# Performance work log

Hardware: AMD Instinct MI355X
Metric: run time of the kernel (lower is better)

Reference implementation:

```python
import jax, jax.numpy as jnp
import numpy as np

IMG_W, IMG_H = 640, 360
STRIDE = 32
S = 72                      # n_offsets
FMAP_H, FMAP_W = IMG_H // STRIDE, IMG_W // STRIDE   # 11, 20
CF = 64                     # anchor_feat_channels
CBACK = 512                 # resnet34 output channels
NP = 4                      # n_proposal
B = 512
F = CF * FMAP_H             # 704


def setup_inputs() -> dict:
    key = jax.random.key(0)
    ks = jax.random.split(key, 8)
    feat = jax.random.normal(ks[0], (B, CBACK, FMAP_H, FMAP_W), dtype=jnp.float32)
    # rpn proposals: (x_px, y_px, unused, angle_deg)
    x = jax.random.uniform(ks[1], (B, NP)) * IMG_W
    y = jax.random.uniform(ks[2], (B, NP)) * IMG_H
    ang = 30.0 + jax.random.uniform(ks[3], (B, NP)) * 120.0   # degrees in [30,150]
    rpn_proposals = jnp.stack([x, y, jnp.zeros_like(x), ang], axis=-1).astype(jnp.float32)
    conv_w = jax.random.normal(ks[4], (CF, CBACK), dtype=jnp.float32) * 0.02
    conv_b = jnp.zeros((CF,), jnp.float32)
    att_w = jax.random.normal(ks[5], (NP - 1, F), dtype=jnp.float32) * 0.02
    att_b = jnp.zeros((NP - 1,), jnp.float32)
    cls_w = jax.random.normal(ks[6], (2, 2 * F), dtype=jnp.float32) * 0.02
    cls_b = jnp.zeros((2,), jnp.float32)
    reg_w = jax.random.normal(ks[7], (S + 1, 2 * F), dtype=jnp.float32) * 0.02
    reg_b = jnp.zeros((S + 1,), jnp.float32)
    return {"feat": feat, "rpn_proposals": rpn_proposals, "conv_w": conv_w,
            "conv_b": conv_b, "att_w": att_w, "att_b": att_b,
            "cls_w": cls_w, "cls_b": cls_b, "reg_w": reg_w, "reg_b": reg_b}


# off-diagonal scatter pattern of the 4x4 attention matrix (row-major order of eye==0)
_ROWS = np.repeat(np.arange(NP), NP - 1)                       # (12,)
_COLS = np.array([j for i in range(NP) for j in range(NP) if j != i])  # (12,)


def reference(feat, rpn_proposals, conv_w, conv_b, att_w, att_b, cls_w, cls_b, reg_w, reg_b):
    bsz = feat.shape[0]
    anchor_ys = jnp.linspace(1.0, 0.0, S)          # (72,)
    anchor_cut_ys = jnp.linspace(1.0, 0.0, FMAP_H) # (11,)

    # --- generate_anchor (vectorized over batch x 4 proposals) ---
    start_x = rpn_proposals[..., 0] / IMG_W        # (B,4)
    start_y = rpn_proposals[..., 1] / IMG_H        # (B,4)
    tan = jnp.tan(rpn_proposals[..., 3] * (np.pi / 180.0))
    xs_full = (start_x[..., None] + (start_y[..., None] - anchor_ys) / tan[..., None]) * IMG_W      # (B,4,72)
    xs_cut = (start_x[..., None] + (start_y[..., None] - anchor_cut_ys) / tan[..., None]) * IMG_W   # (B,4,11)

    anchors = jnp.zeros((bsz, NP, 5 + S), jnp.float32)
    anchors = anchors.at[..., 2].set(1.0 - start_y)
    anchors = anchors.at[..., 3].set(start_x)
    anchors = anchors.at[..., 5:].set(xs_full)

    # --- anchor cut indices (flip along fmap_h like the original) ---
    unclamped = jnp.flip(jnp.round(xs_cut / STRIDE).astype(jnp.int32), axis=-1)  # (B,4,11)
    cut_x = jnp.clip(unclamped, 0, FMAP_W - 1)
    invalid = (unclamped < 0) | (unclamped > FMAP_W)   # faithful: > fmap_w, not >=

    # --- conv1 (1x1 conv) ---
    f = jnp.einsum('bchw,oc->bohw', feat, conv_w) + conv_b[None, :, None, None]  # (B,64,11,20)

    # --- cut_anchor_features: gather f[b, c, y, cut_x[b,p,y]], zero invalid ---
    g = jnp.take_along_axis(f[:, None], cut_x[:, :, None, :, None], axis=4)[..., 0]  # (B,4,64,11)
    g = jnp.where(invalid[:, :, None, :], 0.0, g)
    anchor_feat = g.reshape(bsz, NP, F)  # (B,4,704)

    # --- attention: softmax over 3 non-self anchors, scattered off-diagonal ---
    scores = anchor_feat.reshape(-1, F) @ att_w.T + att_b          # (B*4,3)
    attention = jax.nn.softmax(scores, axis=1).reshape(bsz, NP, NP - 1)
    att_mat = jnp.zeros((bsz, NP, NP), jnp.float32).at[:, _ROWS, _COLS].set(attention.reshape(bsz, -1))

    # attention_features[b,i,:] = sum_j att_mat[b,i,j] * anchor_feat[b,j,:]
    att_feat = jnp.einsum('bij,bjf->bif', att_mat, anchor_feat)    # (B,4,704)
    cat = jnp.concatenate([att_feat, anchor_feat], axis=-1)        # (B,4,1408)

    cls_logits = cat @ cls_w.T + cls_b                             # (B,4,2)
    reg = cat @ reg_w.T + reg_b                                    # (B,4,73)

    reg_proposals = anchors
    reg_proposals = reg_proposals.at[..., :2].set(cls_logits)
    reg_proposals = reg_proposals.at[..., 4:].add(reg)
    # nms(): with conf_threshold=None, anchors[:,:,0]==0 so num_to_keep==4 -> all kept.
    return reg_proposals
```

## Files before the change

### kernel.cpp

```cpp
#include <hip/hip_runtime.h>
#include <math.h>

#define NPROP 4
#define SFULL 72
#define FH 11
#define FW 20
#define CB 512
#define FDIM 704
#define HW 220
#define CHT 32
#define NTILE 16
#define MROWS 160

typedef __attribute__((ext_vector_type(8))) short bf16x8;
typedef __attribute__((ext_vector_type(4))) float f32x4;

__device__ __forceinline__ unsigned short f2bf(float x) {
  unsigned u = __float_as_uint(x);
  u += 0x7FFFu + ((u >> 16) & 1u);
  return (unsigned short)(u >> 16);
}
__device__ __forceinline__ unsigned bfbits(float x) {
  unsigned u = __float_as_uint(x);
  return u + 0x7FFFu + ((u >> 16) & 1u);
}

__device__ __forceinline__ void gload16(const void* g, void* l) {
  __builtin_amdgcn_global_load_lds(
      (const __attribute__((address_space(1))) void*)(g),
      (__attribute__((address_space(3))) void*)(l), 16, 0, 0);
}

__global__ void k_prep(const float* __restrict__ cls_w, const float* __restrict__ reg_w,
                       const float* __restrict__ att_w, const float* __restrict__ conv_w,
                       unsigned short* __restrict__ Wc, unsigned short* __restrict__ Wb2) {
  const int blk = blockIdx.x;
  const int t = threadIdx.x;
  if (blk < MROWS) {
    const int m = blk;
    const float* rowp = nullptr;
    if (m < 150) {
      int o = (m < 75) ? m : m - 75;
      int half = (m < 75) ? 0 : FDIM;
      rowp = ((o < 2) ? (cls_w + o * 2 * FDIM) : (reg_w + (o - 2) * 2 * FDIM)) + half;
    } else if (m < 153) {
      rowp = att_w + (m - 150) * FDIM;
    }
    for (int f = t; f < FDIM; f += 256) {
      float v = rowp ? rowp[f] : 0.0f;
      int fp = (f % FH) * 64 + (f / FH);
      Wc[m * FDIM + fp] = f2bf(v);
    }
  } else {
    const int kg = blk - MROWS;
    #pragma unroll
    for (int e0 = 0; e0 < 2; e0++) {
      int e = t + 256 * e0;
      Wb2[kg * 512 + e] = f2bf(conv_w[(e >> 3) * CB + kg * 8 + (e & 7)]);
    }
  }
}

__global__ __launch_bounds__(512, 4) void k_gconv(
    const float* __restrict__ feat, const float* __restrict__ rpn,
    const unsigned short* __restrict__ Wb2, const float* __restrict__ conv_b,
    unsigned short* __restrict__ af, float* __restrict__ xs_full,
    float* __restrict__ out)
{
  __shared__ __align__(16) unsigned short W2[64 * 512];
  __shared__ __align__(16) unsigned short As[2 * 48 * 40];
  __shared__ float sh_sx[NPROP], sh_sy[NPROP], sh_it[NPROP];
  __shared__ int   sh_pos[48];
  __shared__ int   hcnt[55];
  __shared__ unsigned hword[55];

  const int b = blockIdx.x;
  const int t = threadIdx.x;
  const int l = t & 63;
  const int wid = t >> 6;
  const int nt = wid & 3;
  const int mhalf = wid >> 2;
  const int q = l >> 4, r = l & 15;

  if (t < NPROP) {
    const float* rp = rpn + (b * NPROP + t) * 4;
    float sx = rp[0] * (1.0f / 640.0f);
    float sy = rp[1] * (1.0f / 360.0f);
    float tn = tanf(rp[3] * 0.017453292519943295f);
    sh_sx[t] = sx; sh_sy[t] = sy; sh_it[t] = 1.0f / tn;
    out[(b * NPROP + t) * 77 + 2] = 1.0f - sy;
    out[(b * NPROP + t) * 77 + 3] = sx;
  }
  __syncthreads();
  if (t < NPROP * SFULL) {
    int p = t / SFULL, i = t - p * SFULL;
    float ay = 1.0f - (float)i * (1.0f / 71.0f);
    xs_full[(b * NPROP + p) * SFULL + i] =
        (sh_sx[p] + (sh_sy[p] - ay) * sh_it[p]) * 640.0f;
  }
  if (t < 48) {
    int ps = -1;
    if (t < NPROP * FH) {
      int p = t / FH, y = t - p * FH;
      float acy = 1.0f - (float)(10 - y) * 0.1f;
      float xc = (sh_sx[p] + (sh_sy[p] - acy) * sh_it[p]) * 640.0f;
      int ui = (int)rintf(xc * (1.0f / 32.0f));
      int cut = min(max(ui, 0), FW - 1);
      ps = ((ui < 0) | (ui > FW)) ? -1 : (t % FH) * FW + cut;
    }
    sh_pos[t] = ps;
  }
  __syncthreads();

  if (t < 55) {
    int cnt = 0; unsigned w = 0;
    for (int s = 0; s < 44; s++) {
      int p = sh_pos[s];
      if (p >= 0 && (p >> 2) == t) {
        w |= ((unsigned)(s | ((p & 3) << 6))) << (8 * cnt);
        cnt++;
      }
    }
    hcnt[t] = cnt; hword[t] = w;
  }
  __syncthreads();

  int hn[4]; unsigned hwd[4]; int chS[4]; int cid[4];
  const int cbase = 220 * wid;
  #pragma unroll
  for (int k = 0; k < 4; k++) {
    int c = cbase + 64 * k + l;
    bool ok = (k < 3) || (l < 28);
    cid[k] = c;
    int j = c % 55;
    chS[k] = c / 55;
    hn[k]  = ok ? hcnt[j] : 0;
    hwd[k] = hword[j];
  }

  const float* fb = feat + (size_t)b * (CB * HW);

  #pragma unroll
  for (int k = 0; k < 8; k++) {
    int chunk = t + 512 * k;
    gload16(Wb2 + chunk * 8, (void*)&W2[chunk * 8]);
  }
  __builtin_amdgcn_sched_barrier(0);

  float4 pf[3][4];
  #pragma unroll
  for (int s = 0; s < 3; s++) {
    const float4* g = (const float4*)(fb + s * (CHT * HW));
    #pragma unroll
    for (int k = 0; k < 3; k++) pf[s][k] = g[cid[k]];
    if (l < 28) pf[s][3] = g[cid[3]];
    __builtin_amdgcn_sched_barrier(0);
  }

  f32x4 acc0 = {0.f, 0.f, 0.f, 0.f}, acc1 = {0.f, 0.f, 0.f, 0.f};
  const int cW = 16 * nt + r;

  #pragma unroll
  for (int ct = 0; ct < NTILE; ct++) {
    if (ct <= 13)      asm volatile("s_waitcnt vmcnt(8)" ::: "memory");
    else if (ct == 14) asm volatile("s_waitcnt vmcnt(4)" ::: "memory");
    else               asm volatile("s_waitcnt vmcnt(0)" ::: "memory");
    __builtin_amdgcn_sched_barrier(0);

    unsigned short* Asb = As + (ct & 1) * 1920;
    #pragma unroll
    for (int k = 0; k < 4; k++) {
      int n = hn[k];
      if (n) {
        float4 v4 = pf[ct % 3][k];
        unsigned d0 = (bfbits(v4.x) >> 16) | (bfbits(v4.y) & 0xFFFF0000u);
        unsigned d1 = (bfbits(v4.z) >> 16) | (bfbits(v4.w) & 0xFFFF0000u);
        unsigned wd = hwd[k];
        #pragma unroll
        for (int h = 0; h < 4; h++) {
          if (h < n) {
            unsigned byte = (wd >> (8 * h)) & 255u;
            unsigned s = byte & 63u;
            unsigned sel = (byte & 128u) ? d1 : d0;
            unsigned short val = (byte & 64u) ? (unsigned short)(sel >> 16)
                                              : (unsigned short)sel;
            Asb[s * 40 + chS[k]] = val;
          }
        }
      }
    }
    if (ct + 3 < NTILE) {
      const float4* g = (const float4*)(fb + (ct + 3) * (CHT * HW));
      #pragma unroll
      for (int k = 0; k < 3; k++) pf[ct % 3][k] = g[cid[k]];
      if (l < 28) pf[ct % 3][3] = g[cid[3]];
    }
    asm volatile("s_waitcnt lgkmcnt(0)" ::: "memory");
    __builtin_amdgcn_sched_barrier(0);
    __builtin_amdgcn_s_barrier();
    __builtin_amdgcn_sched_barrier(0);

    bf16x8 bw = *(const bf16x8*)&W2[((ct * 4 + q) * 64 + cW) * 8];
    if (mhalf == 0) {
      bf16x8 a0 = *(const bf16x8*)&Asb[(0 + r) * 40 + q * 8];
      bf16x8 a1 = *(const bf16x8*)&Asb[(16 + r) * 40 + q * 8];
      asm volatile("s_waitcnt lgkmcnt(0)" ::: "memory");
      __builtin_amdgcn_sched_barrier(0);
      acc0 = __builtin_amdgcn_mfma_f32_16x16x32_bf16(a0, bw, acc0, 0, 0, 0);
      acc1 = __builtin_amdgcn_mfma_f32_16x16x32_bf16(a1, bw, acc1, 0, 0, 0);
    } else {
      bf16x8 a2 = *(const bf16x8*)&Asb[(32 + r) * 40 + q * 8];
      asm volatile("s_waitcnt lgkmcnt(0)" ::: "memory");
      __builtin_amdgcn_sched_barrier(0);
      acc0 = __builtin_amdgcn_mfma_f32_16x16x32_bf16(a2, bw, acc0, 0, 0, 0);
    }
  }

  {
    const int c = cW;
    const int g = q;
    const float cb = conv_b[c];
    #pragma unroll
    for (int rr = 0; rr < 4; rr++) {
      if (mhalf == 0) {
        int m0 = g * 4 + rr;
        int p = m0 / FH, y = m0 - p * FH;
        float v = (sh_pos[m0] >= 0) ? (acc0[rr] + cb) : 0.0f;
        af[(size_t)(b * NPROP + p) * FDIM + y * 64 + c] = f2bf(v);
        int m1 = 16 + g * 4 + rr;
        p = m1 / FH; y = m1 - p * FH;
        v = (sh_pos[m1] >= 0) ? (acc1[rr] + cb) : 0.0f;
        af[(size_t)(b * NPROP + p) * FDIM + y * 64 + c] = f2bf(v);
      } else {
        int m2 = 32 + g * 4 + rr;
        if (m2 < 44) {
          int p = m2 / FH, y = m2 - p * FH;
          float v = (sh_pos[m2] >= 0) ? (acc0[rr] + cb) : 0.0f;
          af[(size_t)(b * NPROP + p) * FDIM + y * 64 + c] = f2bf(v);
        }
      }
    }
  }
}

__global__ __launch_bounds__(256) void k_head(
    const unsigned short* __restrict__ af, const float* __restrict__ xs,
    const unsigned short* __restrict__ Wc,
    const float* __restrict__ att_b, const float* __restrict__ cls_b,
    const float* __restrict__ reg_b, float* __restrict__ out)
{
  __shared__ __align__(16) unsigned short A_s[16 * 712];
  __shared__ __align__(16) unsigned short W_s[2][MROWS * 40];
  __shared__ float Ys[16 * 161];
  __shared__ float Am[16][4];

  const int bg = blockIdx.x;
  const int t = threadIdx.x;
  const int l = t & 63;
  const int wid = t >> 6;

  {
    const unsigned* src = (const unsigned*)af + (size_t)bg * 16 * 352;
    for (int i = t; i < 16 * 352; i += 256) {
      int r = i / 352, ci = i - r * 352;
      ((unsigned*)A_s)[r * 356 + ci] = src[i];
    }
  }
  {
    #pragma unroll
    for (int e = t; e < 640; e += 256) {
      int n = e >> 2, jj = e & 3;
      uint4 ld = *(const uint4*)(Wc + n * FDIM + jj * 8);
      *(uint4*)(&W_s[0][n * 40 + jj * 8]) = ld;
    }
  }
  __syncthreads();

  f32x4 acc[3];
  acc[0] = (f32x4){0.f,0.f,0.f,0.f}; acc[1] = acc[0]; acc[2] = acc[0];

  for (int step = 0; step < 22; ++step) {
    int cur = step & 1;
    uint4 r0, r1, r2;
    bool h2 = (t + 512) < 640;
    if (step < 21) {
      int k0 = (step + 1) * 32;
      { int e = t;       int n = e >> 2, jj = e & 3; r0 = *(const uint4*)(Wc + n * FDIM + k0 + jj * 8); }
      { int e = t + 256; int n = e >> 2, jj = e & 3; r1 = *(const uint4*)(Wc + n * FDIM + k0 + jj * 8); }
      if (h2) { int e = t + 512; int n = e >> 2, jj = e & 3; r2 = *(const uint4*)(Wc + n * FDIM + k0 + jj * 8); }
    }
    bf16x8 a = *(const bf16x8*)(A_s + (l & 15) * 712 + step * 32 + (l >> 4) * 8);
    #pragma unroll
    for (int j = 0; j < 3; j++) {
      int ntl = wid + 4 * j;
      if (ntl < 10) {
        bf16x8 bb = *(const bf16x8*)(&W_s[cur][(ntl * 16 + (l & 15)) * 40 + (l >> 4) * 8]);
        acc[j] = __builtin_amdgcn_mfma_f32_16x16x32_bf16(a, bb, acc[j], 0, 0, 0);
      }
    }
    if (step < 21) {
      { int e = t;       int n = e >> 2, jj = e & 3; *(uint4*)(&W_s[cur ^ 1][n * 40 + jj * 8]) = r0; }
      { int e = t + 256; int n = e >> 2, jj = e & 3; *(uint4*)(&W_s[cur ^ 1][n * 40 + jj * 8]) = r1; }
      if (h2) { int e = t + 512; int n = e >> 2, jj = e & 3; *(uint4*)(&W_s[cur ^ 1][n * 40 + jj * 8]) = r2; }
    }
    __syncthreads();
  }

  #pragma unroll
  for (int j = 0; j < 3; j++) {
    int ntl = wid + 4 * j;
    if (ntl < 10) {
      #pragma unroll
      for (int r = 0; r < 4; r++)
        Ys[((l >> 4) * 4 + r) * 161 + ntl * 16 + (l & 15)] = acc[j][r];
    }
  }
  __syncthreads();

  if (t < 16) {
    float s0 = Ys[t * 161 + 150] + att_b[0];
    float s1 = Ys[t * 161 + 151] + att_b[1];
    float s2 = Ys[t * 161 + 152] + att_b[2];
    float mx = fmaxf(s0, fmaxf(s1, s2));
    float e0 = expf(s0 - mx), e1 = expf(s1 - mx), e2 = expf(s2 - mx);
    float inv = 1.0f / (e0 + e1 + e2);
    float aa[3] = {e0 * inv, e1 * inv, e2 * inv};
    int p = t & 3;
    #pragma unroll
    for (int qq = 0; qq < NPROP; qq++)
      Am[t][qq] = (qq == p) ? 0.0f : aa[(qq < p) ? qq : qq - 1];
  }
  __syncthreads();

  for (int d = t; d < 16 * 75; d += 256) {
    int row = d / 75, o = d - row * 75;
    float v = Ys[row * 161 + 75 + o];
    int base = row & ~3;
    #pragma unroll
    for (int qq = 0; qq < NPROP; qq++) v += Am[row][qq] * Ys[(base + qq) * 161 + o];
    v += (o < 2) ? cls_b[o] : reg_b[o - 2];
    int grow = bg * 16 + row;
    int col = (o < 2) ? o : o + 2;
    if (o >= 3) v += xs[grow * SFULL + (o - 3)];
    out[grow * 77 + col] = v;
  }
}

extern "C" void kernel_launch(void* const* d_in, const int* in_sizes, int n_in,
                              void* d_out, int out_size, void* d_ws, size_t ws_size,
                              hipStream_t stream) {
  const float* feat   = (const float*)d_in[0];
  const float* rpn    = (const float*)d_in[1];
  const float* conv_w = (const float*)d_in[2];
  const float* conv_b = (const float*)d_in[3];
  const float* att_w  = (const float*)d_in[4];
  const float* att_b  = (const float*)d_in[5];
  const float* cls_w  = (const float*)d_in[6];
  const float* cls_b  = (const float*)d_in[7];
  const float* reg_w  = (const float*)d_in[8];
  const float* reg_b  = (const float*)d_in[9];
  float* out = (float*)d_out;

  char* ws = (char*)d_ws;
  unsigned short* af  = (unsigned short*)ws;
  float* xs           = (float*)(ws + 2883584);
  unsigned short* Wc  = (unsigned short*)(ws + 2883584 + 589824);
  unsigned short* Wb2 = (unsigned short*)(ws + 2883584 + 589824 + 225280);

  k_prep<<<224, 256, 0, stream>>>(cls_w, reg_w, att_w, conv_w, Wc, Wb2);
  k_gconv<<<512, 512, 0, stream>>>(feat, rpn, Wb2, conv_b, af, xs, out);
  k_head<<<128, 256, 0, stream>>>(af, xs, Wc, att_b, cls_b, reg_b, out);
}
```

Before: 67.42 us.

## Split gconv channel reduction across two blocks per batch with fp32 partials

Each batch element's 512-channel conv reduction is now split into two halves handled by separate blocks, doubling the gconv grid to 1024 blocks and halving per-block LDS weight staging. The two halves write fp32 partial anchor features, which the head kernel sums and converts to bf16 while loading. The head kernel now processes 8 rows per block over 256 blocks. The aim is better occupancy and latency hiding in the memory-bound gather stage. The cost is extra fp32 partial-sum traffic, twice the intermediate bytes, and head blocks whose MFMA tiles are half used.

```diff
diff --git a/kernel.cpp b/kernel.cpp
--- a/kernel.cpp
+++ b/kernel.cpp
@@ -9,7 +9,7 @@
 #define FDIM 704
 #define HW 220
 #define CHT 32
-#define NTILE 16
+#define HTILE 8
 #define MROWS 160
 
 typedef __attribute__((ext_vector_type(8))) short bf16x8;
@@ -64,17 +64,17 @@
 __global__ __launch_bounds__(512, 4) void k_gconv(
     const float* __restrict__ feat, const float* __restrict__ rpn,
     const unsigned short* __restrict__ Wb2, const float* __restrict__ conv_b,
-    unsigned short* __restrict__ af, float* __restrict__ xs_full,
-    float* __restrict__ out)
+    float* __restrict__ af0, float* __restrict__ af1,
+    float* __restrict__ xs_full, float* __restrict__ out)
 {
-  __shared__ __align__(16) unsigned short W2[64 * 512];
-  __shared__ __align__(16) unsigned short As[2 * 48 * 40];
+  __shared__ __align__(16) unsigned short W2[16384];
+  __shared__ __align__(16) unsigned short As[2 * 44 * 40];
   __shared__ float sh_sx[NPROP], sh_sy[NPROP], sh_it[NPROP];
   __shared__ int   sh_pos[48];
-  __shared__ int   hcnt[55];
   __shared__ unsigned hword[55];
 
-  const int b = blockIdx.x;
+  const int b = blockIdx.x >> 1;
+  const int h = blockIdx.x & 1;
   const int t = threadIdx.x;
   const int l = t & 63;
   const int wid = t >> 6;
@@ -88,11 +88,13 @@
     float sy = rp[1] * (1.0f / 360.0f);
     float tn = tanf(rp[3] * 0.017453292519943295f);
     sh_sx[t] = sx; sh_sy[t] = sy; sh_it[t] = 1.0f / tn;
-    out[(b * NPROP + t) * 77 + 2] = 1.0f - sy;
-    out[(b * NPROP + t) * 77 + 3] = sx;
-  }
-  __syncthreads();
-  if (t < NPROP * SFULL) {
+    if (h == 0) {
+      out[(b * NPROP + t) * 77 + 2] = 1.0f - sy;
+      out[(b * NPROP + t) * 77 + 3] = sx;
+    }
+  }
+  __syncthreads();
+  if (h == 0 && t < NPROP * SFULL) {
     int p = t / SFULL, i = t - p * SFULL;
     float ay = 1.0f - (float)i * (1.0f / 71.0f);
     xs_full[(b * NPROP + p) * SFULL + i] =
@@ -113,15 +115,15 @@
   __syncthreads();
 
   if (t < 55) {
-    int cnt = 0; unsigned w = 0;
+    unsigned w = 0; int cnt = 0;
     for (int s = 0; s < 44; s++) {
       int p = sh_pos[s];
       if (p >= 0 && (p >> 2) == t) {
-        w |= ((unsigned)(s | ((p & 3) << 6))) << (8 * cnt);
+        w |= ((unsigned)((s + 1) | ((p & 3) << 6))) << (8 * cnt);
         cnt++;
       }
     }
-    hcnt[t] = cnt; hword[t] = w;
+    hword[t] = w;
   }
   __syncthreads();
 
@@ -132,18 +134,19 @@
     int c = cbase + 64 * k + l;
     bool ok = (k < 3) || (l < 28);
     cid[k] = c;
-    int j = c % 55;
     chS[k] = c / 55;
-    hn[k]  = ok ? hcnt[j] : 0;
-    hwd[k] = hword[j];
-  }
-
-  const float* fb = feat + (size_t)b * (CB * HW);
-
-  #pragma unroll
-  for (int k = 0; k < 8; k++) {
+    unsigned w = hword[c % 55];
+    hwd[k] = w;
+    hn[k]  = (ok && w) ? (4 - (__clz(w) >> 3)) : 0;
+  }
+
+  const float* fb = feat + (size_t)b * (CB * HW) + (size_t)h * (256 * HW);
+  const unsigned short* Wb2h = Wb2 + h * 16384;
+
+  #pragma unroll
+  for (int k = 0; k < 4; k++) {
     int chunk = t + 512 * k;
-    gload16(Wb2 + chunk * 8, (void*)&W2[chunk * 8]);
+    gload16(Wb2h + chunk * 8, (void*)&W2[chunk * 8]);
   }
   __builtin_amdgcn_sched_barrier(0);
 
@@ -161,13 +164,13 @@
   const int cW = 16 * nt + r;
 
   #pragma unroll
-  for (int ct = 0; ct < NTILE; ct++) {
-    if (ct <= 13)      asm volatile("s_waitcnt vmcnt(8)" ::: "memory");
-    else if (ct == 14) asm volatile("s_waitcnt vmcnt(4)" ::: "memory");
-    else               asm volatile("s_waitcnt vmcnt(0)" ::: "memory");
+  for (int ct = 0; ct < HTILE; ct++) {
+    if (ct <= 5)      asm volatile("s_waitcnt vmcnt(8)" ::: "memory");
+    else if (ct == 6) asm volatile("s_waitcnt vmcnt(4)" ::: "memory");
+    else              asm volatile("s_waitcnt vmcnt(0)" ::: "memory");
     __builtin_amdgcn_sched_barrier(0);
 
-    unsigned short* Asb = As + (ct & 1) * 1920;
+    unsigned short* Asb = As + (ct & 1) * 1760;
     #pragma unroll
     for (int k = 0; k < 4; k++) {
       int n = hn[k];
@@ -177,10 +180,10 @@
         unsigned d1 = (bfbits(v4.z) >> 16) | (bfbits(v4.w) & 0xFFFF0000u);
         unsigned wd = hwd[k];
         #pragma unroll
-        for (int h = 0; h < 4; h++) {
-          if (h < n) {
-            unsigned byte = (wd >> (8 * h)) & 255u;
-            unsigned s = byte & 63u;
+        for (int hh = 0; hh < 4; hh++) {
+          if (hh < n) {
+            unsigned byte = (wd >> (8 * hh)) & 255u;
+            unsigned s = (byte & 63u) - 1u;
             unsigned sel = (byte & 128u) ? d1 : d0;
             unsigned short val = (byte & 64u) ? (unsigned short)(sel >> 16)
                                               : (unsigned short)sel;
@@ -189,7 +192,7 @@
         }
       }
     }
-    if (ct + 3 < NTILE) {
+    if (ct + 3 < HTILE) {
       const float4* g = (const float4*)(fb + (ct + 3) * (CHT * HW));
       #pragma unroll
       for (int k = 0; k < 3; k++) pf[ct % 3][k] = g[cid[k]];
@@ -217,26 +220,27 @@
   }
 
   {
+    float* afh = h ? af1 : af0;
     const int c = cW;
     const int g = q;
-    const float cb = conv_b[c];
+    const float cb = (h == 0) ? conv_b[c] : 0.0f;
     #pragma unroll
     for (int rr = 0; rr < 4; rr++) {
       if (mhalf == 0) {
         int m0 = g * 4 + rr;
         int p = m0 / FH, y = m0 - p * FH;
         float v = (sh_pos[m0] >= 0) ? (acc0[rr] + cb) : 0.0f;
-        af[(size_t)(b * NPROP + p) * FDIM + y * 64 + c] = f2bf(v);
+        afh[(size_t)(b * NPROP + p) * FDIM + y * 64 + c] = v;
         int m1 = 16 + g * 4 + rr;
         p = m1 / FH; y = m1 - p * FH;
         v = (sh_pos[m1] >= 0) ? (acc1[rr] + cb) : 0.0f;
-        af[(size_t)(b * NPROP + p) * FDIM + y * 64 + c] = f2bf(v);
+        afh[(size_t)(b * NPROP + p) * FDIM + y * 64 + c] = v;
       } else {
         int m2 = 32 + g * 4 + rr;
         if (m2 < 44) {
           int p = m2 / FH, y = m2 - p * FH;
           float v = (sh_pos[m2] >= 0) ? (acc0[rr] + cb) : 0.0f;
-          af[(size_t)(b * NPROP + p) * FDIM + y * 64 + c] = f2bf(v);
+          afh[(size_t)(b * NPROP + p) * FDIM + y * 64 + c] = v;
         }
       }
     }
@@ -244,15 +248,15 @@
 }
 
 __global__ __launch_bounds__(256) void k_head(
-    const unsigned short* __restrict__ af, const float* __restrict__ xs,
-    const unsigned short* __restrict__ Wc,
+    const float* __restrict__ af0, const float* __restrict__ af1,
+    const float* __restrict__ xs, const unsigned short* __restrict__ Wc,
     const float* __restrict__ att_b, const float* __restrict__ cls_b,
     const float* __restrict__ reg_b, float* __restrict__ out)
 {
   __shared__ __align__(16) unsigned short A_s[16 * 712];
   __shared__ __align__(16) unsigned short W_s[2][MROWS * 40];
   __shared__ float Ys[16 * 161];
-  __shared__ float Am[16][4];
+  __shared__ float Am[8][4];
 
   const int bg = blockIdx.x;
   const int t = threadIdx.x;
@@ -260,10 +264,15 @@
   const int wid = t >> 6;
 
   {
-    const unsigned* src = (const unsigned*)af + (size_t)bg * 16 * 352;
-    for (int i = t; i < 16 * 352; i += 256) {
-      int r = i / 352, ci = i - r * 352;
-      ((unsigned*)A_s)[r * 356 + ci] = src[i];
+    const float4* s0 = (const float4*)(af0 + (size_t)bg * 8 * FDIM);
+    const float4* s1 = (const float4*)(af1 + (size_t)bg * 8 * FDIM);
+    for (int i = t; i < 1408; i += 256) {
+      float4 a = s0[i], c = s1[i];
+      unsigned lo = (bfbits(a.x + c.x) >> 16) | (bfbits(a.y + c.y) & 0xFFFF0000u);
+      unsigned hi = (bfbits(a.z + c.z) >> 16) | (bfbits(a.w + c.w) & 0xFFFF0000u);
+      int row = i / 176, c4 = i - row * 176;
+      uint2 pk; pk.x = lo; pk.y = hi;
+      *(uint2*)(A_s + row * 712 + c4 * 4) = pk;
     }
   }
   {
@@ -317,7 +326,7 @@
   }
   __syncthreads();
 
-  if (t < 16) {
+  if (t < 8) {
     float s0 = Ys[t * 161 + 150] + att_b[0];
     float s1 = Ys[t * 161 + 151] + att_b[1];
     float s2 = Ys[t * 161 + 152] + att_b[2];
@@ -332,14 +341,14 @@
   }
   __syncthreads();
 
-  for (int d = t; d < 16 * 75; d += 256) {
+  for (int d = t; d < 8 * 75; d += 256) {
     int row = d / 75, o = d - row * 75;
     float v = Ys[row * 161 + 75 + o];
     int base = row & ~3;
     #pragma unroll
     for (int qq = 0; qq < NPROP; qq++) v += Am[row][qq] * Ys[(base + qq) * 161 + o];
     v += (o < 2) ? cls_b[o] : reg_b[o - 2];
-    int grow = bg * 16 + row;
+    int grow = bg * 8 + row;
     int col = (o < 2) ? o : o + 2;
     if (o >= 3) v += xs[grow * SFULL + (o - 3)];
     out[grow * 77 + col] = v;
@@ -362,12 +371,13 @@
   float* out = (float*)d_out;
 
   char* ws = (char*)d_ws;
-  unsigned short* af  = (unsigned short*)ws;
-  float* xs           = (float*)(ws + 2883584);
-  unsigned short* Wc  = (unsigned short*)(ws + 2883584 + 589824);
-  unsigned short* Wb2 = (unsigned short*)(ws + 2883584 + 589824 + 225280);
+  float* af0 = (float*)ws;
+  float* af1 = (float*)(ws + 5767168);
+  float* xs  = (float*)(ws + 11534336);
+  unsigned short* Wc  = (unsigned short*)(ws + 12124160);
+  unsigned short* Wb2 = (unsigned short*)(ws + 12349440);
 
   k_prep<<<224, 256, 0, stream>>>(cls_w, reg_w, att_w, conv_w, Wc, Wb2);
-  k_gconv<<<512, 512, 0, stream>>>(feat, rpn, Wb2, conv_b, af, xs, out);
-  k_head<<<128, 256, 0, stream>>>(af, xs, Wc, att_b, cls_b, reg_b, out);
-}
+  k_gconv<<<1024, 512, 0, stream>>>(feat, rpn, Wb2, conv_b, af0, af1, xs, out);
+  k_head<<<256, 256, 0, stream>>>(af0, af1, xs, Wc, att_b, cls_b, reg_b, out);
+}
```

Result: slower. 68.89 us (+2.2%).

## Split gconv K across waves with register-resident conv weights and LDS reduction

Applied to the files above, without the earlier changes.

The gather-conv kernel now runs 256 threads per block. Each wave owns a 128-channel slice of the K dimension and computes all 48x64 outputs with conv weights converted to bf16 straight into registers, which removes the separate weight-prep pass and the LDS weight staging. The per-tile block barriers are gone, and feature loads are streamed per wave through an 8-deep register prefetch. Partial sums are reduced across waves through LDS with a serialized loop before the bias, mask and store. The costs are more register pressure, each block re-reading and converting conv_w from global memory, and a serialized four-step reduction.

```diff
diff --git a/kernel.cpp b/kernel.cpp
--- a/kernel.cpp
+++ b/kernel.cpp
@@ -8,8 +8,6 @@
 #define CB 512
 #define FDIM 704
 #define HW 220
-#define CHT 32
-#define NTILE 16
 #define MROWS 160
 
 typedef __attribute__((ext_vector_type(8))) short bf16x8;
@@ -25,61 +23,41 @@
   return u + 0x7FFFu + ((u >> 16) & 1u);
 }
 
-__device__ __forceinline__ void gload16(const void* g, void* l) {
-  __builtin_amdgcn_global_load_lds(
-      (const __attribute__((address_space(1))) void*)(g),
-      (__attribute__((address_space(3))) void*)(l), 16, 0, 0);
-}
-
 __global__ void k_prep(const float* __restrict__ cls_w, const float* __restrict__ reg_w,
-                       const float* __restrict__ att_w, const float* __restrict__ conv_w,
-                       unsigned short* __restrict__ Wc, unsigned short* __restrict__ Wb2) {
-  const int blk = blockIdx.x;
+                       const float* __restrict__ att_w, unsigned short* __restrict__ Wc) {
+  const int m = blockIdx.x;
   const int t = threadIdx.x;
-  if (blk < MROWS) {
-    const int m = blk;
-    const float* rowp = nullptr;
-    if (m < 150) {
-      int o = (m < 75) ? m : m - 75;
-      int half = (m < 75) ? 0 : FDIM;
-      rowp = ((o < 2) ? (cls_w + o * 2 * FDIM) : (reg_w + (o - 2) * 2 * FDIM)) + half;
-    } else if (m < 153) {
-      rowp = att_w + (m - 150) * FDIM;
-    }
-    for (int f = t; f < FDIM; f += 256) {
-      float v = rowp ? rowp[f] : 0.0f;
-      int fp = (f % FH) * 64 + (f / FH);
-      Wc[m * FDIM + fp] = f2bf(v);
-    }
-  } else {
-    const int kg = blk - MROWS;
-    #pragma unroll
-    for (int e0 = 0; e0 < 2; e0++) {
-      int e = t + 256 * e0;
-      Wb2[kg * 512 + e] = f2bf(conv_w[(e >> 3) * CB + kg * 8 + (e & 7)]);
-    }
-  }
-}
-
-__global__ __launch_bounds__(512, 4) void k_gconv(
+  const float* rowp = nullptr;
+  if (m < 150) {
+    int o = (m < 75) ? m : m - 75;
+    int half = (m < 75) ? 0 : FDIM;
+    rowp = ((o < 2) ? (cls_w + o * 2 * FDIM) : (reg_w + (o - 2) * 2 * FDIM)) + half;
+  } else if (m < 153) {
+    rowp = att_w + (m - 150) * FDIM;
+  }
+  for (int f = t; f < FDIM; f += 256) {
+    float v = rowp ? rowp[f] : 0.0f;
+    int fp = (f % FH) * 64 + (f / FH);
+    Wc[m * FDIM + fp] = f2bf(v);
+  }
+}
+
+__global__ __launch_bounds__(256, 2) void k_gconv(
     const float* __restrict__ feat, const float* __restrict__ rpn,
-    const unsigned short* __restrict__ Wb2, const float* __restrict__ conv_b,
+    const float* __restrict__ conv_w, const float* __restrict__ conv_b,
     unsigned short* __restrict__ af, float* __restrict__ xs_full,
     float* __restrict__ out)
 {
-  __shared__ __align__(16) unsigned short W2[64 * 512];
-  __shared__ __align__(16) unsigned short As[2 * 48 * 40];
+  __shared__ __align__(16) unsigned short As[4][48 * 40];
+  __shared__ float Rbuf[48 * 65];
   __shared__ float sh_sx[NPROP], sh_sy[NPROP], sh_it[NPROP];
   __shared__ int   sh_pos[48];
-  __shared__ int   hcnt[55];
   __shared__ unsigned hword[55];
 
   const int b = blockIdx.x;
   const int t = threadIdx.x;
   const int l = t & 63;
   const int wid = t >> 6;
-  const int nt = wid & 3;
-  const int mhalf = wid >> 2;
   const int q = l >> 4, r = l & 15;
 
   if (t < NPROP) {
@@ -92,10 +70,10 @@
     out[(b * NPROP + t) * 77 + 3] = sx;
   }
   __syncthreads();
-  if (t < NPROP * SFULL) {
-    int p = t / SFULL, i = t - p * SFULL;
-    float ay = 1.0f - (float)i * (1.0f / 71.0f);
-    xs_full[(b * NPROP + p) * SFULL + i] =
+  for (int i = t; i < NPROP * SFULL; i += 256) {
+    int p = i / SFULL, k = i - p * SFULL;
+    float ay = 1.0f - (float)k * (1.0f / 71.0f);
+    xs_full[(b * NPROP + p) * SFULL + k] =
         (sh_sx[p] + (sh_sy[p] - ay) * sh_it[p]) * 640.0f;
   }
   if (t < 48) {
@@ -111,135 +89,134 @@
     sh_pos[t] = ps;
   }
   __syncthreads();
-
   if (t < 55) {
-    int cnt = 0; unsigned w = 0;
+    unsigned w = 0; int cnt = 0;
     for (int s = 0; s < 44; s++) {
       int p = sh_pos[s];
       if (p >= 0 && (p >> 2) == t) {
-        w |= ((unsigned)(s | ((p & 3) << 6))) << (8 * cnt);
+        w |= ((unsigned)((s + 1) | ((p & 3) << 6))) << (8 * cnt);
         cnt++;
       }
     }
-    hcnt[t] = cnt; hword[t] = w;
-  }
-  __syncthreads();
-
-  int hn[4]; unsigned hwd[4]; int chS[4]; int cid[4];
-  const int cbase = 220 * wid;
-  #pragma unroll
-  for (int k = 0; k < 4; k++) {
-    int c = cbase + 64 * k + l;
-    bool ok = (k < 3) || (l < 28);
-    cid[k] = c;
-    int j = c % 55;
-    chS[k] = c / 55;
-    hn[k]  = ok ? hcnt[j] : 0;
-    hwd[k] = hword[j];
-  }
-
-  const float* fb = feat + (size_t)b * (CB * HW);
-
-  #pragma unroll
-  for (int k = 0; k < 8; k++) {
-    int chunk = t + 512 * k;
-    gload16(Wb2 + chunk * 8, (void*)&W2[chunk * 8]);
-  }
+    hword[t] = w;
+  }
+  __syncthreads();
+
+  bf16x8 bfr[4][4];
+  #pragma unroll
+  for (int s = 0; s < 4; s++) {
+    #pragma unroll
+    for (int j = 0; j < 4; j++) {
+      const float* p = conv_w + (16 * j + r) * CB + 128 * wid + 32 * s + 8 * q;
+      float4 u = *(const float4*)p;
+      float4 v = *(const float4*)(p + 4);
+      bfr[s][j][0] = (short)f2bf(u.x); bfr[s][j][1] = (short)f2bf(u.y);
+      bfr[s][j][2] = (short)f2bf(u.z); bfr[s][j][3] = (short)f2bf(u.w);
+      bfr[s][j][4] = (short)f2bf(v.x); bfr[s][j][5] = (short)f2bf(v.y);
+      bfr[s][j][6] = (short)f2bf(v.z); bfr[s][j][7] = (short)f2bf(v.w);
+    }
+  }
+
+  const float4* f4 = (const float4*)(feat + (size_t)b * (CB * HW) + wid * (128 * HW));
+  const int l55m = (l < 55) ? l : l - 55;
+  const int l55S = (l < 55) ? 0 : 1;
+
+  asm volatile("s_waitcnt vmcnt(0)" ::: "memory");
   __builtin_amdgcn_sched_barrier(0);
 
-  float4 pf[3][4];
-  #pragma unroll
-  for (int s = 0; s < 3; s++) {
-    const float4* g = (const float4*)(fb + s * (CHT * HW));
-    #pragma unroll
-    for (int k = 0; k < 3; k++) pf[s][k] = g[cid[k]];
-    if (l < 28) pf[s][3] = g[cid[3]];
-    __builtin_amdgcn_sched_barrier(0);
-  }
-
-  f32x4 acc0 = {0.f, 0.f, 0.f, 0.f}, acc1 = {0.f, 0.f, 0.f, 0.f};
-  const int cW = 16 * nt + r;
-
-  #pragma unroll
-  for (int ct = 0; ct < NTILE; ct++) {
-    if (ct <= 13)      asm volatile("s_waitcnt vmcnt(8)" ::: "memory");
-    else if (ct == 14) asm volatile("s_waitcnt vmcnt(4)" ::: "memory");
-    else               asm volatile("s_waitcnt vmcnt(0)" ::: "memory");
-    __builtin_amdgcn_sched_barrier(0);
-
-    unsigned short* Asb = As + (ct & 1) * 1920;
-    #pragma unroll
-    for (int k = 0; k < 4; k++) {
-      int n = hn[k];
-      if (n) {
-        float4 v4 = pf[ct % 3][k];
-        unsigned d0 = (bfbits(v4.x) >> 16) | (bfbits(v4.y) & 0xFFFF0000u);
-        unsigned d1 = (bfbits(v4.z) >> 16) | (bfbits(v4.w) & 0xFFFF0000u);
-        unsigned wd = hwd[k];
-        #pragma unroll
-        for (int h = 0; h < 4; h++) {
-          if (h < n) {
-            unsigned byte = (wd >> (8 * h)) & 255u;
-            unsigned s = byte & 63u;
-            unsigned sel = (byte & 128u) ? d1 : d0;
-            unsigned short val = (byte & 64u) ? (unsigned short)(sel >> 16)
-                                              : (unsigned short)sel;
-            Asb[s * 40 + chS[k]] = val;
+  float4 pf[8];
+  #pragma unroll
+  for (int g = 0; g < 7; g++) {
+    const int s2 = g / 28, i2 = g % 28;
+    int c = 64 * i2 + l; if (i2 == 27) c = (c < 1760) ? c : 1759;
+    pf[g & 7] = f4[s2 * 1760 + c];
+  }
+
+  f32x4 acc[3][4];
+  #pragma unroll
+  for (int mt = 0; mt < 3; mt++)
+    #pragma unroll
+    for (int j = 0; j < 4; j++) acc[mt][j] = (f32x4){0.f, 0.f, 0.f, 0.f};
+
+  unsigned short* AsW = As[wid];
+
+  #pragma unroll
+  for (int s = 0; s < 4; s++) {
+    int m = l55m, S = l55S;
+    #pragma unroll
+    for (int i = 0; i < 28; i++) {
+      const int g = 28 * s + i;
+      {
+        const int gi = (g + 7 < 112) ? (g + 7) : 111;
+        const int s2 = gi / 28, i2 = gi % 28;
+        int c = 64 * i2 + l; if (i2 == 27) c = (c < 1760) ? c : 1759;
+        pf[(g + 7) & 7] = f4[s2 * 1760 + c];
+      }
+      asm volatile("s_waitcnt vmcnt(7)" ::: "memory");
+      __builtin_amdgcn_sched_barrier(0);
+
+      if (S < 32) {
+        unsigned w = hword[m];
+        if (w) {
+          float4 v4 = pf[g & 7];
+          unsigned d0 = (bfbits(v4.x) >> 16) | (bfbits(v4.y) & 0xFFFF0000u);
+          unsigned d1 = (bfbits(v4.z) >> 16) | (bfbits(v4.w) & 0xFFFF0000u);
+          int n = 4 - (__clz(w) >> 3);
+          #pragma unroll
+          for (int h = 0; h < 4; h++) {
+            if (h < n) {
+              unsigned byte = (w >> (8 * h)) & 255u;
+              unsigned row = (byte & 63u) - 1u;
+              unsigned sel = (byte & 128u) ? d1 : d0;
+              unsigned short val = (byte & 64u) ? (unsigned short)(sel >> 16)
+                                                : (unsigned short)sel;
+              AsW[row * 40 + S] = val;
+            }
           }
         }
       }
-    }
-    if (ct + 3 < NTILE) {
-      const float4* g = (const float4*)(fb + (ct + 3) * (CHT * HW));
-      #pragma unroll
-      for (int k = 0; k < 3; k++) pf[ct % 3][k] = g[cid[k]];
-      if (l < 28) pf[ct % 3][3] = g[cid[3]];
-    }
+      m += 9; S += 1;
+      if (m >= 55) { m -= 55; S += 1; }
+    }
+
     asm volatile("s_waitcnt lgkmcnt(0)" ::: "memory");
     __builtin_amdgcn_sched_barrier(0);
-    __builtin_amdgcn_s_barrier();
+    bf16x8 a0 = *(const bf16x8*)&AsW[(0 + r) * 40 + q * 8];
+    bf16x8 a1 = *(const bf16x8*)&AsW[(16 + r) * 40 + q * 8];
+    bf16x8 a2 = *(const bf16x8*)&AsW[(32 + r) * 40 + q * 8];
+    asm volatile("s_waitcnt lgkmcnt(0)" ::: "memory");
     __builtin_amdgcn_sched_barrier(0);
-
-    bf16x8 bw = *(const bf16x8*)&W2[((ct * 4 + q) * 64 + cW) * 8];
-    if (mhalf == 0) {
-      bf16x8 a0 = *(const bf16x8*)&Asb[(0 + r) * 40 + q * 8];
-      bf16x8 a1 = *(const bf16x8*)&Asb[(16 + r) * 40 + q * 8];
-      asm volatile("s_waitcnt lgkmcnt(0)" ::: "memory");
-      __builtin_amdgcn_sched_barrier(0);
-      acc0 = __builtin_amdgcn_mfma_f32_16x16x32_bf16(a0, bw, acc0, 0, 0, 0);
-      acc1 = __builtin_amdgcn_mfma_f32_16x16x32_bf16(a1, bw, acc1, 0, 0, 0);
-    } else {
-      bf16x8 a2 = *(const bf16x8*)&Asb[(32 + r) * 40 + q * 8];
-      asm volatile("s_waitcnt lgkmcnt(0)" ::: "memory");
-      __builtin_amdgcn_sched_barrier(0);
-      acc0 = __builtin_amdgcn_mfma_f32_16x16x32_bf16(a2, bw, acc0, 0, 0, 0);
-    }
-  }
-
-  {
-    const int c = cW;
-    const int g = q;
-    const float cb = conv_b[c];
-    #pragma unroll
-    for (int rr = 0; rr < 4; rr++) {
-      if (mhalf == 0) {
-        int m0 = g * 4 + rr;
-        int p = m0 / FH, y = m0 - p * FH;
-        float v = (sh_pos[m0] >= 0) ? (acc0[rr] + cb) : 0.0f;
-        af[(size_t)(b * NPROP + p) * FDIM + y * 64 + c] = f2bf(v);
-        int m1 = 16 + g * 4 + rr;
-        p = m1 / FH; y = m1 - p * FH;
-        v = (sh_pos[m1] >= 0) ? (acc1[rr] + cb) : 0.0f;
-        af[(size_t)(b * NPROP + p) * FDIM + y * 64 + c] = f2bf(v);
-      } else {
-        int m2 = 32 + g * 4 + rr;
-        if (m2 < 44) {
-          int p = m2 / FH, y = m2 - p * FH;
-          float v = (sh_pos[m2] >= 0) ? (acc0[rr] + cb) : 0.0f;
-          af[(size_t)(b * NPROP + p) * FDIM + y * 64 + c] = f2bf(v);
+    #pragma unroll
+    for (int j = 0; j < 4; j++) {
+      acc[0][j] = __builtin_amdgcn_mfma_f32_16x16x32_bf16(a0, bfr[s][j], acc[0][j], 0, 0, 0);
+      acc[1][j] = __builtin_amdgcn_mfma_f32_16x16x32_bf16(a1, bfr[s][j], acc[1][j], 0, 0, 0);
+      acc[2][j] = __builtin_amdgcn_mfma_f32_16x16x32_bf16(a2, bfr[s][j], acc[2][j], 0, 0, 0);
+    }
+  }
+
+  for (int w = 0; w < 4; w++) {
+    if (wid == w) {
+      #pragma unroll
+      for (int mt = 0; mt < 3; mt++) {
+        #pragma unroll
+        for (int j = 0; j < 4; j++) {
+          #pragma unroll
+          for (int rr = 0; rr < 4; rr++) {
+            int idx = (16 * mt + 4 * q + rr) * 65 + 16 * j + r;
+            if (w == 0) Rbuf[idx] = acc[mt][j][rr];
+            else        Rbuf[idx] += acc[mt][j][rr];
+          }
         }
       }
     }
+    __syncthreads();
+  }
+
+  for (int e = t; e < 44 * 64; e += 256) {
+    int row = e >> 6, col = e & 63;
+    float v = (sh_pos[row] >= 0) ? (Rbuf[row * 65 + col] + conv_b[col]) : 0.0f;
+    int p = row / FH, y = row - p * FH;
+    af[(size_t)(b * NPROP + p) * FDIM + y * 64 + col] = f2bf(v);
   }
 }
 
@@ -362,12 +339,11 @@
   float* out = (float*)d_out;
 
   char* ws = (char*)d_ws;
-  unsigned short* af  = (unsigned short*)ws;
-  float* xs           = (float*)(ws + 2883584);
-  unsigned short* Wc  = (unsigned short*)(ws + 2883584 + 589824);
-  unsigned short* Wb2 = (unsigned short*)(ws + 2883584 + 589824 + 225280);
-
-  k_prep<<<224, 256, 0, stream>>>(cls_w, reg_w, att_w, conv_w, Wc, Wb2);
-  k_gconv<<<512, 512, 0, stream>>>(feat, rpn, Wb2, conv_b, af, xs, out);
+  unsigned short* af = (unsigned short*)ws;
+  float* xs          = (float*)(ws + 2883584);
+  unsigned short* Wc = (unsigned short*)(ws + 2883584 + 589824);
+
+  k_prep<<<MROWS, 256, 0, stream>>>(cls_w, reg_w, att_w, Wc);
+  k_gconv<<<512, 256, 0, stream>>>(feat, rpn, conv_w, conv_b, af, xs, out);
   k_head<<<128, 256, 0, stream>>>(af, xs, Wc, att_b, cls_b, reg_b, out);
 }
```

New measurement: 95.60 us. 41.8% more time.

## Triple-buffer LDS A tiles and defer MFMA by one tile

Applied to the files above, without the earlier changes.

The A staging buffer goes from two to three buffers, each holding 44 rows instead of 48. The MFMA for tile ct-1 now runs after the barrier of tile ct, so the global-to-LDS scatter of the next tile overlaps the matrix work of the previous one. This keeps one barrier per iteration while removing the write-after-read hazard that double buffering would have. The cost is a slightly longer loop tail and reads of rows 44-47 spilling past each 44-row buffer into the next one, which is only safe if those rows are never stored.

```diff
diff --git a/kernel.cpp b/kernel.cpp
--- a/kernel.cpp
+++ b/kernel.cpp
@@ -68,7 +68,7 @@
     float* __restrict__ out)
 {
   __shared__ __align__(16) unsigned short W2[64 * 512];
-  __shared__ __align__(16) unsigned short As[2 * 48 * 40];
+  __shared__ __align__(16) unsigned short As[3 * 44 * 40];
   __shared__ float sh_sx[NPROP], sh_sy[NPROP], sh_it[NPROP];
   __shared__ int   sh_pos[48];
   __shared__ int   hcnt[55];
@@ -160,6 +160,23 @@
   f32x4 acc0 = {0.f, 0.f, 0.f, 0.f}, acc1 = {0.f, 0.f, 0.f, 0.f};
   const int cW = 16 * nt + r;
 
+#define MFMA_STEP(pt) { \
+    const unsigned short* Asp = As + ((pt) % 3) * 1760; \
+    bf16x8 bw = *(const bf16x8*)&W2[(((pt) * 4 + q) * 64 + cW) * 8]; \
+    if (mhalf == 0) { \
+      bf16x8 a0 = *(const bf16x8*)&Asp[(0 + r) * 40 + q * 8]; \
+      bf16x8 a1 = *(const bf16x8*)&Asp[(16 + r) * 40 + q * 8]; \
+      asm volatile("s_waitcnt lgkmcnt(0)" ::: "memory"); \
+      __builtin_amdgcn_sched_barrier(0); \
+      acc0 = __builtin_amdgcn_mfma_f32_16x16x32_bf16(a0, bw, acc0, 0, 0, 0); \
+      acc1 = __builtin_amdgcn_mfma_f32_16x16x32_bf16(a1, bw, acc1, 0, 0, 0); \
+    } else { \
+      bf16x8 a2 = *(const bf16x8*)&Asp[(32 + r) * 40 + q * 8]; \
+      asm volatile("s_waitcnt lgkmcnt(0)" ::: "memory"); \
+      __builtin_amdgcn_sched_barrier(0); \
+      acc0 = __builtin_amdgcn_mfma_f32_16x16x32_bf16(a2, bw, acc0, 0, 0, 0); \
+    } }
+
   #pragma unroll
   for (int ct = 0; ct < NTILE; ct++) {
     if (ct <= 13)      asm volatile("s_waitcnt vmcnt(8)" ::: "memory");
@@ -167,7 +184,7 @@
     else               asm volatile("s_waitcnt vmcnt(0)" ::: "memory");
     __builtin_amdgcn_sched_barrier(0);
 
-    unsigned short* Asb = As + (ct & 1) * 1920;
+    unsigned short* Asb = As + (ct % 3) * 1760;
     #pragma unroll
     for (int k = 0; k < 4; k++) {
       int n = hn[k];
@@ -200,21 +217,10 @@
     __builtin_amdgcn_s_barrier();
     __builtin_amdgcn_sched_barrier(0);
 
-    bf16x8 bw = *(const bf16x8*)&W2[((ct * 4 + q) * 64 + cW) * 8];
-    if (mhalf == 0) {
-      bf16x8 a0 = *(const bf16x8*)&Asb[(0 + r) * 40 + q * 8];
-      bf16x8 a1 = *(const bf16x8*)&Asb[(16 + r) * 40 + q * 8];
-      asm volatile("s_waitcnt lgkmcnt(0)" ::: "memory");
-      __builtin_amdgcn_sched_barrier(0);
-      acc0 = __builtin_amdgcn_mfma_f32_16x16x32_bf16(a0, bw, acc0, 0, 0, 0);
-      acc1 = __builtin_amdgcn_mfma_f32_16x16x32_bf16(a1, bw, acc1, 0, 0, 0);
-    } else {
-      bf16x8 a2 = *(const bf16x8*)&Asb[(32 + r) * 40 + q * 8];
-      asm volatile("s_waitcnt lgkmcnt(0)" ::: "memory");
-      __builtin_amdgcn_sched_barrier(0);
-      acc0 = __builtin_amdgcn_mfma_f32_16x16x32_bf16(a2, bw, acc0, 0, 0, 0);
-    }
-  }
+    if (ct > 0) MFMA_STEP(ct - 1)
+  }
+  MFMA_STEP(15)
+#undef MFMA_STEP
 
   {
     const int c = cW;
```

Result: no change. 68.75 us (+2.0%).
